# Kernel tuning notes

Hardware: AMD Instinct MI355X
Metric: run time of the kernel (lower is better)

## Reference

```python
import jax, jax.numpy as jnp
import numpy as np

K = 3        # cubic spline degree (hardcoded in module: self.k = 3)
N_KNOTS = 5  # n_knots


def _deboor_np(x, t, c, k):
    """Vectorized de Boor evaluation in numpy (used only to build the
    collocation matrix replicating scipy.splrep interpolation)."""
    m = np.clip(np.searchsorted(t, x, side='right') - 1, k, len(t) - k - 2)
    d = [c[m - k + j] for j in range(k + 1)]
    for r in range(1, k + 1):
        for j in range(k, r - 1, -1):
            left = t[j + m - k]
            right = t[j + 1 + m - r]
            denom = right - left
            safe = np.where(denom > 0, denom, 1.0)
            alpha = np.where(denom > 0, (x - left) / safe, 0.0)
            d[j] = (1.0 - alpha) * d[j - 1] + alpha * d[j]
    return d[k]


def setup_inputs() -> dict:
    key = jax.random.key(0)
    rng = np.random.default_rng(0)
    x_kn = np.linspace(0.0, 1.0, N_KNOTS)
    y_kn = rng.random(N_KNOTS)
    y_kn[0] = 0.0
    y_kn[-1] = 1.0
    # FITPACK interpolation knot layout for n=5, k=3: clamped ends + interior knot at x[2]
    t = np.concatenate([np.zeros(K + 1), x_kn[2:-2], np.ones(K + 1)]).astype(np.float64)
    # collocation matrix A[j, i] = B_i(x_j); solve A c = y  (splrep with s=0)
    eye = np.eye(N_KNOTS)
    A = np.stack([_deboor_np(x_kn, t, eye[i], K) for i in range(N_KNOTS)], axis=1)
    c = np.linalg.solve(A, y_kn)
    imgs = jax.random.uniform(key, (64, 3, 512, 512), dtype=jnp.float32)
    return {
        "imgs": imgs,
        "t": jnp.asarray(t, dtype=jnp.float32),
        "c": jnp.asarray(c, dtype=jnp.float32),
    }


def reference(imgs, t, c):
    """Elementwise cubic B-spline evaluation of imgs via de Boor's recursion,
    then zero-masking where the input was exactly zero (as in the torch module)."""
    k = K
    # interval index: t[m] <= x < t[m+1], clamped so boundary/extrapolation
    # uses the edge polynomial (matches scipy BSpline extrapolate=True)
    m = jnp.clip(jnp.searchsorted(t, imgs, side='right') - 1, k, t.shape[0] - k - 2)
    d = [c[m - k + j] for j in range(k + 1)]  # k+1 local coefficients per pixel
    for r in range(1, k + 1):
        for j in range(k, r - 1, -1):
            left = t[j + m - k]
            right = t[j + 1 + m - r]
            denom = right - left
            safe = jnp.where(denom > 0, denom, 1.0)
            alpha = jnp.where(denom > 0, (imgs - left) / safe, 0.0)
            d[j] = (1.0 - alpha) * d[j - 1] + alpha * d[j]
    out = d[k]
    return jnp.where(imgs == 0, jnp.zeros((), dtype=out.dtype), out)
```

## Files before the change

kernel.cpp:

```cpp
#include <hip/hip_runtime.h>


typedef float v4f __attribute__((ext_vector_type(4)));

template<int M>
__device__ inline void expand_piece(const float tt[9], const float cc[5],
                                    float out[4]) {
    float P[4][4];
#pragma unroll
    for (int j = 0; j < 4; ++j) {
        P[j][0] = cc[M - 3 + j];
        P[j][1] = 0.f; P[j][2] = 0.f; P[j][3] = 0.f;
    }
#pragma unroll
    for (int r = 1; r <= 3; ++r) {
#pragma unroll
        for (int j = 3; j >= 1; --j) {
            if (j < r) continue;
            const float L   = tt[j + M - 3];
            const float R   = tt[j + 1 + M - r];
            const float den = R - L;
            const float rd  = den > 0.f ? 1.f / den : 0.f;
            const float p = rd;
            const float q = -rd * L;
            const float e0 = P[j][0] - P[j-1][0];
            const float e1 = P[j][1] - P[j-1][1];
            const float e2 = P[j][2] - P[j-1][2];
            const float e3 = P[j][3] - P[j-1][3];
            P[j][0] = P[j-1][0] + q * e0;
            P[j][1] = P[j-1][1] + q * e1 + p * e0;
            P[j][2] = P[j-1][2] + q * e2 + p * e1;
            P[j][3] = P[j-1][3] + q * e3 + p * e2;
        }
    }
#pragma unroll
    for (int i = 0; i < 4; ++i) out[i] = P[3][i];
}

__global__ __launch_bounds__(256) void bspline_kernel(
    const v4f* __restrict__ in4,
    v4f* __restrict__ out4,
    const float* __restrict__ t,
    const float* __restrict__ c,
    int n4)
{
    float tt[9], cc[5];
#pragma unroll
    for (int i = 0; i < 9; ++i) tt[i] = t[i];
#pragma unroll
    for (int i = 0; i < 5; ++i) cc[i] = c[i];

    float A[4], B[4];
    expand_piece<3>(tt, cc, A);
    expand_piece<4>(tt, cc, B);
    const float t4 = tt[4];

    auto eval = [&](float x) -> float {
        const bool up = (x >= t4);
        const float k0 = up ? B[0] : A[0];
        const float k1 = up ? B[1] : A[1];
        const float k2 = up ? B[2] : A[2];
        const float k3 = up ? B[3] : A[3];
        float y = fmaf(fmaf(fmaf(k3, x, k2), x, k1), x, k0);
        return (x == 0.f) ? 0.f : y;
    };

    const int tid    = blockIdx.x * (blockDim.x * 2) + threadIdx.x;
    const int stride = gridDim.x * blockDim.x * 2;

    for (int i0 = tid; i0 < n4; i0 += stride) {
        const int i1 = i0 + blockDim.x;
        v4f v0 = __builtin_nontemporal_load(&in4[i0]);
        v4f v1;
        const bool has1 = (i1 < n4);
        if (has1) v1 = __builtin_nontemporal_load(&in4[i1]);

        v4f o0, o1;
        o0.x = eval(v0.x); o0.y = eval(v0.y);
        o0.z = eval(v0.z); o0.w = eval(v0.w);
        __builtin_nontemporal_store(o0, &out4[i0]);

        if (has1) {
            o1.x = eval(v1.x); o1.y = eval(v1.y);
            o1.z = eval(v1.z); o1.w = eval(v1.w);
            __builtin_nontemporal_store(o1, &out4[i1]);
        }
    }
}

extern "C" void kernel_launch(void* const* d_in, const int* in_sizes, int n_in,
                              void* d_out, int out_size, void* d_ws, size_t ws_size,
                              hipStream_t stream) {
    const float* imgs = (const float*)d_in[0];
    const float* t    = (const float*)d_in[1];
    const float* c    = (const float*)d_in[2];
    float* out = (float*)d_out;

    const int n  = in_sizes[0];
    const int n4 = n / 4;

    const int block = 256;
    int grid = 8192;
    int max_grid = (n4 + block * 2 - 1) / (block * 2);
    if (grid > max_grid) grid = max_grid;

    bspline_kernel<<<grid, block, 0, stream>>>(
        (const v4f*)imgs, (v4f*)out, t, c, n4);
}
```

Baseline: 319.2 us.

## Precompute spline polynomial coefficients in setup kernel and use one-shot unrolled blocks

Moves the per-thread expansion of the two cubic pieces into a tiny single-thread setup kernel that writes the coefficients to workspace, so the main kernel only loads nine scalars. The main kernel drops the grid-stride loop in favour of one block per 4x256 float4 chunk, with all loads issued before compute. Input loads are now regular (temporal) rather than nontemporal. This adds a second kernel launch and a dependency on workspace, in exchange for less per-thread setup arithmetic and more memory-level parallelism per thread.

```diff
diff --git a/kernel.cpp b/kernel.cpp
--- a/kernel.cpp
+++ b/kernel.cpp
@@ -4,7 +4,7 @@
 typedef float v4f __attribute__((ext_vector_type(4)));
 
 template<int M>
-__device__ inline void expand_piece(const float tt[9], const float cc[5],
+__device__ inline void expand_piece(const float* tt, const float* cc,
                                     float out[4]) {
     float P[4][4];
 #pragma unroll
@@ -37,53 +37,66 @@
     for (int i = 0; i < 4; ++i) out[i] = P[3][i];
 }
 
-__global__ __launch_bounds__(256) void bspline_kernel(
+__global__ void setup_kernel(const float* __restrict__ t,
+                             const float* __restrict__ c,
+                             float* __restrict__ ws) {
+    if (threadIdx.x == 0) {
+        float A[4], B[4];
+        expand_piece<3>(t, c, A);
+        expand_piece<4>(t, c, B);
+        ws[0] = A[0]; ws[1] = A[1]; ws[2] = A[2]; ws[3] = A[3];
+        ws[4] = B[0]; ws[5] = B[1]; ws[6] = B[2]; ws[7] = B[3];
+        ws[8] = t[4];
+    }
+}
+
+#define UNROLL 4
+
+__global__ __launch_bounds__(256) void bspline_main(
     const v4f* __restrict__ in4,
     v4f* __restrict__ out4,
-    const float* __restrict__ t,
-    const float* __restrict__ c,
-    int n4)
+    const float* __restrict__ ws,
+    int n4, int fullBlocks)
 {
-    float tt[9], cc[5];
-#pragma unroll
-    for (int i = 0; i < 9; ++i) tt[i] = t[i];
-#pragma unroll
-    for (int i = 0; i < 5; ++i) cc[i] = c[i];
-
-    float A[4], B[4];
-    expand_piece<3>(tt, cc, A);
-    expand_piece<4>(tt, cc, B);
-    const float t4 = tt[4];
+    const float A0 = ws[0], A1 = ws[1], A2 = ws[2], A3 = ws[3];
+    const float B0 = ws[4], B1 = ws[5], B2 = ws[6], B3 = ws[7];
+    const float t4 = ws[8];
 
     auto eval = [&](float x) -> float {
         const bool up = (x >= t4);
-        const float k0 = up ? B[0] : A[0];
-        const float k1 = up ? B[1] : A[1];
-        const float k2 = up ? B[2] : A[2];
-        const float k3 = up ? B[3] : A[3];
+        const float k0 = up ? B0 : A0;
+        const float k1 = up ? B1 : A1;
+        const float k2 = up ? B2 : A2;
+        const float k3 = up ? B3 : A3;
         float y = fmaf(fmaf(fmaf(k3, x, k2), x, k1), x, k0);
         return (x == 0.f) ? 0.f : y;
     };
 
-    const int tid    = blockIdx.x * (blockDim.x * 2) + threadIdx.x;
-    const int stride = gridDim.x * blockDim.x * 2;
+    const int base = blockIdx.x * (256 * UNROLL) + (int)threadIdx.x;
 
-    for (int i0 = tid; i0 < n4; i0 += stride) {
-        const int i1 = i0 + blockDim.x;
-        v4f v0 = __builtin_nontemporal_load(&in4[i0]);
-        v4f v1;
-        const bool has1 = (i1 < n4);
-        if (has1) v1 = __builtin_nontemporal_load(&in4[i1]);
-
-        v4f o0, o1;
-        o0.x = eval(v0.x); o0.y = eval(v0.y);
-        o0.z = eval(v0.z); o0.w = eval(v0.w);
-        __builtin_nontemporal_store(o0, &out4[i0]);
-
-        if (has1) {
-            o1.x = eval(v1.x); o1.y = eval(v1.y);
-            o1.z = eval(v1.z); o1.w = eval(v1.w);
-            __builtin_nontemporal_store(o1, &out4[i1]);
+    if (blockIdx.x < fullBlocks) {
+        v4f v[UNROLL];
+#pragma unroll
+        for (int u = 0; u < UNROLL; ++u)
+            v[u] = in4[base + u * 256];
+#pragma unroll
+        for (int u = 0; u < UNROLL; ++u) {
+            v4f o;
+            o.x = eval(v[u].x); o.y = eval(v[u].y);
+            o.z = eval(v[u].z); o.w = eval(v[u].w);
+            __builtin_nontemporal_store(o, &out4[base + u * 256]);
+        }
+    } else {
+#pragma unroll
+        for (int u = 0; u < UNROLL; ++u) {
+            const int i = base + u * 256;
+            if (i < n4) {
+                v4f v = in4[i];
+                v4f o;
+                o.x = eval(v.x); o.y = eval(v.y);
+                o.z = eval(v.z); o.w = eval(v.w);
+                __builtin_nontemporal_store(o, &out4[i]);
+            }
         }
     }
 }
@@ -95,15 +108,16 @@
     const float* t    = (const float*)d_in[1];
     const float* c    = (const float*)d_in[2];
     float* out = (float*)d_out;
+    float* ws  = (float*)d_ws;
 
     const int n  = in_sizes[0];
     const int n4 = n / 4;
+    const int perBlock   = 256 * UNROLL;
+    const int fullBlocks = n4 / perBlock;
+    const int rem        = n4 - fullBlocks * perBlock;
+    const int grid       = fullBlocks + (rem ? 1 : 0);
 
-    const int block = 256;
-    int grid = 8192;
-    int max_grid = (n4 + block * 2 - 1) / (block * 2);
-    if (grid > max_grid) grid = max_grid;
-
-    bspline_kernel<<<grid, block, 0, stream>>>(
-        (const v4f*)imgs, (v4f*)out, t, c, n4);
+    setup_kernel<<<1, 64, 0, stream>>>(t, c, ws);
+    bspline_main<<<grid, 256, 0, stream>>>(
+        (const v4f*)imgs, (v4f*)out, ws, n4, fullBlocks);
 }
```

After: 341.7 us. 7.0% more time.
